# Kernel optimization log

Measured on AMD Instinct MI355X. Metric: run time of the kernel, lower is better.

The kernel has to match this reference:

```python
import jax, jax.numpy as jnp
import numpy as np

B, S, D, H = 2, 2048, 1024, 16
HD = D // H  # head_dim = 64
ROPE_BASE = 10000.0


def setup_inputs() -> dict:
    key = jax.random.key(0)
    ks = jax.random.split(key, 5)
    scale = 1.0 / np.sqrt(D)
    return {
        "x": jax.random.normal(ks[0], (B, S, D), dtype=jnp.float32),
        "Wq": jax.random.normal(ks[1], (D, D), dtype=jnp.float32) * scale,
        "Wk": jax.random.normal(ks[2], (D, D), dtype=jnp.float32) * scale,
        "Wv": jax.random.normal(ks[3], (D, D), dtype=jnp.float32) * scale,
        "Wo": jax.random.normal(ks[4], (D, D), dtype=jnp.float32) * scale,
    }


def _rotate_half(x):
    x1, x2 = x[..., : HD // 2], x[..., HD // 2:]
    return jnp.concatenate((-x2, x1), axis=-1)


def _rope_cos_sin(seq_len):
    inv_freq = 1.0 / (ROPE_BASE ** (jnp.arange(0, HD, 2, dtype=jnp.float32) / HD))
    t = jnp.arange(seq_len, dtype=jnp.float32)
    freqs = jnp.outer(t, inv_freq)          # [S, HD/2]
    emb = jnp.concatenate((freqs, freqs), -1)  # [S, HD]
    return jnp.cos(emb), jnp.sin(emb)


def reference(x, Wq, Wk, Wv, Wo):
    # projections (torch Linear: y = x @ W.T), split heads -> [B, H, S, HD]
    def proj(W):
        return (x @ W.T).reshape(B, S, H, HD).transpose(0, 2, 1, 3)

    q, k, v = proj(Wq), proj(Wk), proj(Wv)

    cos, sin = _rope_cos_sin(S)  # [S, HD] each, broadcast over B, H
    q = q * cos + _rotate_half(q) * sin
    k = k * cos + _rotate_half(k) * sin

    scale = 1.0 / np.sqrt(HD)
    scores = jnp.einsum("bhsd,bhtd->bhst", q, k) * scale  # [B,H,S,S]
    attn = jax.nn.softmax(scores, axis=-1)
    out = jnp.einsum("bhst,bhtd->bhsd", attn, v)           # [B,H,S,HD]
    out = out.transpose(0, 2, 1, 3).reshape(B, S, D)
    return out @ Wo.T
```

## Files before the change

kernel.cpp:

```cpp
#include <hip/hip_runtime.h>
#include <hip/hip_bf16.h>
#include <math.h>
#include <stdint.h>

typedef __bf16 bf16;
typedef __bf16 bf16x8 __attribute__((ext_vector_type(8)));
typedef __bf16 bf16x4 __attribute__((ext_vector_type(4)));
typedef float  f32x4  __attribute__((ext_vector_type(4)));

#define MFMA16(a,b,c) __builtin_amdgcn_mfma_f32_16x16x32_bf16((a),(b),(c),0,0,0)
#define GLOAD_LDS16(g, l) \
  __builtin_amdgcn_global_load_lds((__attribute__((address_space(1))) void*)(g), \
                                   (__attribute__((address_space(3))) void*)(l), 16, 0, 0)

static constexpr int kB  = 2;
static constexpr int kS  = 2048;
static constexpr int kD  = 1024;
static constexpr int kH  = 16;
static constexpr int kHD = 64;
static constexpr int kM  = kB * kS;
static constexpr float kExpC = 0.125f * 1.44269504f;

__global__ void cvt_all(const float* __restrict__ x,
                        const float* __restrict__ wq, const float* __restrict__ wk,
                        const float* __restrict__ wv, const float* __restrict__ wo,
                        bf16* __restrict__ xb,
                        bf16* __restrict__ wqb, bf16* __restrict__ wkb,
                        bf16* __restrict__ wvb, bf16* __restrict__ wob,
                        float2* __restrict__ rtab)
{
  const int i = blockIdx.x * 256 + threadIdx.x;
  const int NX4 = (kM * kD) / 4;
  const int NW4 = (kD * kD) / 4;
  if (i >= NX4 + 4 * NW4) {
    const int idx = i - (NX4 + 4 * NW4);
    const int s = idx >> 5, d = idx & 31;
    const float f = exp2f(-(float)d * 0.4152410118609203f);
    float sn, cs;
    sincosf((float)s * f, &sn, &cs);
    rtab[idx] = make_float2(cs, sn);
    return;
  }
  const float* src; bf16* dst; int off;
  if (i < NX4) { src = x; dst = xb; off = i; }
  else {
    const int j = i - NX4;
    const int seg = j >> 18;
    off = j & (NW4 - 1);
    src = (seg == 0) ? wq : (seg == 1) ? wk : (seg == 2) ? wv : wo;
    dst = (seg == 0) ? wqb : (seg == 1) ? wkb : (seg == 2) ? wvb : wob;
  }
  const float4 v = ((const float4*)src)[off];
  bf16x4 o = { (bf16)v.x, (bf16)v.y, (bf16)v.z, (bf16)v.w };
  ((bf16x4*)dst)[off] = o;
}

__device__ __forceinline__ void gemm_core_128(
    const bf16* __restrict__ A, const bf16* __restrict__ Bw,
    int m0, int n0, int K, bf16* aT, bf16* bT, f32x4 acc[4][4])
{
  const int t = threadIdx.x, lane = t & 63, wave = t >> 6;
  const int wm = wave >> 1, wn = wave & 1;
  const int srow = lane >> 2;
  const int scol = (lane & 3) * 8;
  for (int k0 = 0; k0 < K; k0 += 32) {
    __syncthreads();
#pragma unroll
    for (int c = 0; c < 2; ++c) {
      const int row = c * 64 + wave * 16 + srow;
      const bf16* ga = A  + (size_t)(m0 + row) * K + k0 + scol;
      const bf16* gb = Bw + (size_t)(n0 + row) * K + k0 + scol;
      GLOAD_LDS16(ga, aT + c * 2048 + wave * 512);
      GLOAD_LDS16(gb, bT + c * 2048 + wave * 512);
    }
    __syncthreads();
    bf16x8 af[4], bfr[4];
#pragma unroll
    for (int i = 0; i < 4; ++i) {
      af[i]  = *(const bf16x8*)(aT + (wm * 64 + i * 16 + (lane & 15)) * 32 + (lane >> 4) * 8);
      bfr[i] = *(const bf16x8*)(bT + (wn * 64 + i * 16 + (lane & 15)) * 32 + (lane >> 4) * 8);
    }
#pragma unroll
    for (int i = 0; i < 4; ++i)
#pragma unroll
      for (int j = 0; j < 4; ++j)
        acc[i][j] = MFMA16(af[i], bfr[j], acc[i][j]);
  }
}

__global__ __launch_bounds__(256) void proj_qkv(
    const bf16* __restrict__ xb,
    const bf16* __restrict__ wqb, const bf16* __restrict__ wkb, const bf16* __restrict__ wvb,
    bf16* __restrict__ Qb, bf16* __restrict__ Kb, bf16* __restrict__ Vb,
    const float2* __restrict__ rtab)
{
  __shared__ __align__(16) bf16 aT[4096];
  __shared__ __align__(16) bf16 bT[4096];
  const int z = blockIdx.z;
  const bf16* Ww = (z == 0) ? wqb : (z == 1) ? wkb : wvb;
  bf16*       Op = (z == 0) ? Qb  : (z == 1) ? Kb  : Vb;
  const int m0 = blockIdx.x * 128, n0 = blockIdx.y * 128;
  f32x4 acc[4][4] = {};
  gemm_core_128(xb, Ww, m0, n0, kD, aT, bT, acc);

  const int lane = threadIdx.x & 63, wave = threadIdx.x >> 6;
  const int wm = wave >> 1, wn = wave & 1, quad = lane >> 4, lc = lane & 15;
  const int hh = (n0 >> 6) + wn;
  if (z == 2) {
#pragma unroll
    for (int i = 0; i < 4; ++i)
#pragma unroll
      for (int r = 0; r < 4; ++r) {
        const int m = m0 + wm * 64 + i * 16 + quad * 4 + r;
        const int bidx = m >> 11, s = m & 2047;
        bf16* dst = Op + ((size_t)(bidx * kH + hh) * kS + s) * kHD;
#pragma unroll
        for (int j = 0; j < 4; ++j) dst[j * 16 + lc] = (bf16)acc[i][j][r];
      }
  } else {
#pragma unroll
    for (int j = 0; j < 2; ++j) {
      const int d = j * 16 + lc;
#pragma unroll
      for (int i = 0; i < 4; ++i)
#pragma unroll
        for (int r = 0; r < 4; ++r) {
          const int m = m0 + wm * 64 + i * 16 + quad * 4 + r;
          const int bidx = m >> 11, s = m & 2047;
          const float2 cs = rtab[s * 32 + d];
          const float v0 = acc[i][j][r], v1 = acc[i][j + 2][r];
          bf16* dst = Op + ((size_t)(bidx * kH + hh) * kS + s) * kHD;
          dst[d]      = (bf16)(v0 * cs.x - v1 * cs.y);
          dst[d + 32] = (bf16)(v1 * cs.x + v0 * cs.y);
        }
    }
  }
}

__global__ __launch_bounds__(256, 2) void attn(
    const bf16* __restrict__ Qb, const bf16* __restrict__ Kb,
    const bf16* __restrict__ Vb, bf16* __restrict__ Ob)
{
  __shared__ __align__(16) bf16 kT[128 * 72];
  __shared__ __align__(16) bf16 vT[64 * 136];
  __shared__ __align__(16) bf16 pT[4][32 * 136];
  const int t = threadIdx.x, lane = t & 63, wave = t >> 6;
  const int quad = lane >> 4, lc = lane & 15;
  const int qt = blockIdx.x, bh = blockIdx.y;
  const size_t base = (size_t)bh * kS * kHD;
  const bf16* Qp = Qb + base + (size_t)qt * 128 * kHD;
  const bf16* Kp = Kb + base;
  const bf16* Vp = Vb + base;

  bf16x8 qf[2][2];
#pragma unroll
  for (int tm = 0; tm < 2; ++tm)
#pragma unroll
    for (int ks = 0; ks < 2; ++ks)
      qf[tm][ks] = *(const bf16x8*)(Qp + (wave * 32 + tm * 16 + lc) * kHD + ks * 32 + quad * 8);

  f32x4 oacc[2][4] = {};
  f32x4 lacc[2] = {};
  const bf16 one = (bf16)1.0f;
  const bf16x8 ones = { one, one, one, one, one, one, one, one };

  const int srow = t >> 1;
  const int shalf = (t & 1) * 32;

  for (int kt = 0; kt < kS / 128; ++kt) {
    __syncthreads();
    {
      const bf16* ksrc = Kp + (size_t)(kt * 128 + srow) * kHD + shalf;
#pragma unroll
      for (int u = 0; u < 4; ++u)
        *(uint4*)&kT[srow * 72 + shalf + u * 8] = *(const uint4*)(ksrc + u * 8);
      const bf16* vsrc = Vp + (size_t)(kt * 128 + srow) * kHD + shalf;
      bf16 tmp[32];
#pragma unroll
      for (int u = 0; u < 4; ++u)
        *(uint4*)&tmp[u * 8] = *(const uint4*)(vsrc + u * 8);
#pragma unroll
      for (int e = 0; e < 32; ++e)
        vT[(shalf + e) * 136 + srow] = tmp[e];
    }
    __syncthreads();

    f32x4 sc[2][8] = {};
#pragma unroll
    for (int nk = 0; nk < 8; ++nk) {
      const bf16x8 kf0 = *(const bf16x8*)&kT[(nk * 16 + lc) * 72 + quad * 8];
      const bf16x8 kf1 = *(const bf16x8*)&kT[(nk * 16 + lc) * 72 + 32 + quad * 8];
#pragma unroll
      for (int tm = 0; tm < 2; ++tm) {
        sc[tm][nk] = MFMA16(qf[tm][0], kf0, sc[tm][nk]);
        sc[tm][nk] = MFMA16(qf[tm][1], kf1, sc[tm][nk]);
      }
    }

    bf16* pw = &pT[wave][0];
#pragma unroll
    for (int tm = 0; tm < 2; ++tm)
#pragma unroll
      for (int nk = 0; nk < 8; ++nk)
#pragma unroll
        for (int r = 0; r < 4; ++r) {
          const float p = __builtin_amdgcn_exp2f(sc[tm][nk][r] * kExpC);
          pw[(tm * 16 + quad * 4 + r) * 136 + nk * 16 + lc] = (bf16)p;
        }

    bf16x8 pf[2][4];
#pragma unroll
    for (int tm = 0; tm < 2; ++tm)
#pragma unroll
      for (int ks = 0; ks < 4; ++ks)
        pf[tm][ks] = *(const bf16x8*)&pw[(tm * 16 + lc) * 136 + ks * 32 + quad * 8];
#pragma unroll
    for (int ks = 0; ks < 4; ++ks)
#pragma unroll
      for (int tm = 0; tm < 2; ++tm)
        lacc[tm] = MFMA16(pf[tm][ks], ones, lacc[tm]);
#pragma unroll
    for (int nd = 0; nd < 4; ++nd)
#pragma unroll
      for (int ks = 0; ks < 4; ++ks) {
        const bf16x8 vf = *(const bf16x8*)&vT[(nd * 16 + lc) * 136 + ks * 32 + quad * 8];
#pragma unroll
        for (int tm = 0; tm < 2; ++tm)
          oacc[tm][nd] = MFMA16(pf[tm][ks], vf, oacc[tm][nd]);
      }
  }

  const int b = bh >> 4, h = bh & 15;
#pragma unroll
  for (int tm = 0; tm < 2; ++tm)
#pragma unroll
    for (int r = 0; r < 4; ++r) {
      const float inv = 1.0f / lacc[tm][r];
      const int s = qt * 128 + wave * 32 + tm * 16 + quad * 4 + r;
      bf16* dst = Ob + ((size_t)(b * kS + s)) * kD + h * kHD;
#pragma unroll
      for (int nd = 0; nd < 4; ++nd)
        dst[nd * 16 + lc] = (bf16)(oacc[tm][nd][r] * inv);
    }
}

__global__ __launch_bounds__(256) void out_proj(
    const bf16* __restrict__ Ab, const bf16* __restrict__ wob, float* __restrict__ Cout)
{
  __shared__ __align__(16) bf16 aT[4096];
  __shared__ __align__(16) bf16 bT[4096];
  const int m0 = blockIdx.x * 128, n0 = blockIdx.y * 128;
  f32x4 acc[4][4] = {};
  gemm_core_128(Ab, wob, m0, n0, kD, aT, bT, acc);
  const int lane = threadIdx.x & 63, wave = threadIdx.x >> 6;
  const int wm = wave >> 1, wn = wave & 1, quad = lane >> 4, lc = lane & 15;
#pragma unroll
  for (int i = 0; i < 4; ++i)
#pragma unroll
    for (int r = 0; r < 4; ++r) {
      const int m = m0 + wm * 64 + i * 16 + quad * 4 + r;
#pragma unroll
      for (int j = 0; j < 4; ++j)
        Cout[(size_t)m * kD + n0 + wn * 64 + j * 16 + lc] = acc[i][j][r];
    }
}

extern "C" void kernel_launch(void* const* d_in, const int* in_sizes, int n_in,
                              void* d_out, int out_size, void* d_ws, size_t ws_size,
                              hipStream_t stream)
{
  const float* x  = (const float*)d_in[0];
  const float* wq = (const float*)d_in[1];
  const float* wk = (const float*)d_in[2];
  const float* wv = (const float*)d_in[3];
  const float* wo = (const float*)d_in[4];
  float* out = (float*)d_out;

  char* ws = (char*)d_ws;
  const size_t MB = 1024 * 1024;
  if (ws_size < 49 * MB) return;
  bf16* xb  = (bf16*)(ws + 0 * MB);
  bf16* wqb = (bf16*)(ws + 8 * MB);
  bf16* wkb = (bf16*)(ws + 10 * MB);
  bf16* wvb = (bf16*)(ws + 12 * MB);
  bf16* wob = (bf16*)(ws + 14 * MB);
  bf16* Qb  = (bf16*)(ws + 16 * MB);
  bf16* Kb  = (bf16*)(ws + 24 * MB);
  bf16* Vb  = (bf16*)(ws + 32 * MB);
  bf16* Ob  = (bf16*)(ws + 40 * MB);
  float2* rtab = (float2*)(ws + 48 * MB);

  cvt_all<<<8448, 256, 0, stream>>>(x, wq, wk, wv, wo, xb, wqb, wkb, wvb, wob, rtab);
  proj_qkv<<<dim3(32, 8, 3), 256, 0, stream>>>(xb, wqb, wkb, wvb, Qb, Kb, Vb, rtab);
  attn<<<dim3(16, 32), 256, 0, stream>>>(Qb, Kb, Vb, Ob);
  out_proj<<<dim3(32, 8), 256, 0, stream>>>(Ob, wob, out);
}
```

Baseline: 215.8 us.

## Pre-transpose V in a separate kernel, fold softmax scale into Q, swap MFMA operands

Adds a transpose_v kernel that writes V as [bh, HD, S] so the attention loop loads V tiles with straight 16-byte copies instead of a 32-element scalar scatter transpose into LDS. The softmax scale times log2(e) is folded into Q at projection time, removing a multiply per score. The QK MFMA operands are swapped so each lane holds 4 consecutive keys and can store P as one bf16x4 vector instead of scalar stores. The cost is one extra kernel launch plus an extra read and write of V through a new 8 MB workspace region.

```diff
diff --git a/kernel.cpp b/kernel.cpp
--- a/kernel.cpp
+++ b/kernel.cpp
@@ -118,6 +118,7 @@
         for (int j = 0; j < 4; ++j) dst[j * 16 + lc] = (bf16)acc[i][j][r];
       }
   } else {
+    const float f = (z == 0) ? kExpC : 1.0f;
 #pragma unroll
     for (int j = 0; j < 2; ++j) {
       const int d = j * 16 + lc;
@@ -130,16 +131,42 @@
           const float2 cs = rtab[s * 32 + d];
           const float v0 = acc[i][j][r], v1 = acc[i][j + 2][r];
           bf16* dst = Op + ((size_t)(bidx * kH + hh) * kS + s) * kHD;
-          dst[d]      = (bf16)(v0 * cs.x - v1 * cs.y);
-          dst[d + 32] = (bf16)(v1 * cs.x + v0 * cs.y);
+          dst[d]      = (bf16)((v0 * cs.x - v1 * cs.y) * f);
+          dst[d + 32] = (bf16)((v1 * cs.x + v0 * cs.y) * f);
         }
     }
+  }
+}
+
+__global__ __launch_bounds__(256) void transpose_v(
+    const bf16* __restrict__ Vb, bf16* __restrict__ Vt)
+{
+  __shared__ __align__(16) bf16 buf[128 * 72];
+  const int t = threadIdx.x;
+  const int kc = blockIdx.x, bh = blockIdx.y;
+  const bf16* src = Vb + ((size_t)bh * kS + kc * 128) * kHD;
+  {
+    const int srow = t >> 1, half = (t & 1) * 32;
+#pragma unroll
+    for (int u = 0; u < 4; ++u)
+      *(uint4*)&buf[srow * 72 + half + u * 8] = *(const uint4*)(src + srow * kHD + half + u * 8);
+  }
+  __syncthreads();
+  {
+    const int d = t & 63, c = t >> 6;
+    bf16 tmp[32];
+#pragma unroll
+    for (int e = 0; e < 32; ++e) tmp[e] = buf[(c * 32 + e) * 72 + d];
+    bf16* dst = Vt + ((size_t)bh * kHD + d) * kS + kc * 128 + c * 32;
+#pragma unroll
+    for (int u = 0; u < 4; ++u)
+      *(uint4*)(dst + u * 8) = *(const uint4*)&tmp[u * 8];
   }
 }
 
 __global__ __launch_bounds__(256, 2) void attn(
     const bf16* __restrict__ Qb, const bf16* __restrict__ Kb,
-    const bf16* __restrict__ Vb, bf16* __restrict__ Ob)
+    const bf16* __restrict__ Vt, bf16* __restrict__ Ob)
 {
   __shared__ __align__(16) bf16 kT[128 * 72];
   __shared__ __align__(16) bf16 vT[64 * 136];
@@ -150,7 +177,7 @@
   const size_t base = (size_t)bh * kS * kHD;
   const bf16* Qp = Qb + base + (size_t)qt * 128 * kHD;
   const bf16* Kp = Kb + base;
-  const bf16* Vp = Vb + base;
+  const bf16* Vp = Vt + base;
 
   bf16x8 qf[2][2];
 #pragma unroll
@@ -164,8 +191,8 @@
   const bf16 one = (bf16)1.0f;
   const bf16x8 ones = { one, one, one, one, one, one, one, one };
 
-  const int srow = t >> 1;
-  const int shalf = (t & 1) * 32;
+  const int srow = t >> 1, shalf = (t & 1) * 32;
+  const int vd = t >> 2, vc = t & 3;
 
   for (int kt = 0; kt < kS / 128; ++kt) {
     __syncthreads();
@@ -174,14 +201,10 @@
 #pragma unroll
       for (int u = 0; u < 4; ++u)
         *(uint4*)&kT[srow * 72 + shalf + u * 8] = *(const uint4*)(ksrc + u * 8);
-      const bf16* vsrc = Vp + (size_t)(kt * 128 + srow) * kHD + shalf;
-      bf16 tmp[32];
+      const bf16* vsrc = Vp + (size_t)vd * kS + kt * 128 + vc * 32;
 #pragma unroll
       for (int u = 0; u < 4; ++u)
-        *(uint4*)&tmp[u * 8] = *(const uint4*)(vsrc + u * 8);
-#pragma unroll
-      for (int e = 0; e < 32; ++e)
-        vT[(shalf + e) * 136 + srow] = tmp[e];
+        *(uint4*)&vT[vd * 136 + vc * 32 + u * 8] = *(const uint4*)(vsrc + u * 8);
     }
     __syncthreads();
 
@@ -192,8 +215,8 @@
       const bf16x8 kf1 = *(const bf16x8*)&kT[(nk * 16 + lc) * 72 + 32 + quad * 8];
 #pragma unroll
       for (int tm = 0; tm < 2; ++tm) {
-        sc[tm][nk] = MFMA16(qf[tm][0], kf0, sc[tm][nk]);
-        sc[tm][nk] = MFMA16(qf[tm][1], kf1, sc[tm][nk]);
+        sc[tm][nk] = MFMA16(kf0, qf[tm][0], sc[tm][nk]);
+        sc[tm][nk] = MFMA16(kf1, qf[tm][1], sc[tm][nk]);
       }
     }
 
@@ -201,12 +224,13 @@
 #pragma unroll
     for (int tm = 0; tm < 2; ++tm)
 #pragma unroll
-      for (int nk = 0; nk < 8; ++nk)
-#pragma unroll
-        for (int r = 0; r < 4; ++r) {
-          const float p = __builtin_amdgcn_exp2f(sc[tm][nk][r] * kExpC);
-          pw[(tm * 16 + quad * 4 + r) * 136 + nk * 16 + lc] = (bf16)p;
-        }
+      for (int nk = 0; nk < 8; ++nk) {
+        bf16x4 p;
+#pragma unroll
+        for (int r = 0; r < 4; ++r)
+          p[r] = (bf16)__builtin_amdgcn_exp2f(sc[tm][nk][r]);
+        *(bf16x4*)&pw[(tm * 16 + lc) * 136 + nk * 16 + quad * 4] = p;
+      }
 
     bf16x8 pf[2][4];
 #pragma unroll
@@ -278,7 +302,7 @@
 
   char* ws = (char*)d_ws;
   const size_t MB = 1024 * 1024;
-  if (ws_size < 49 * MB) return;
+  if (ws_size < 57 * MB) return;
   bf16* xb  = (bf16*)(ws + 0 * MB);
   bf16* wqb = (bf16*)(ws + 8 * MB);
   bf16* wkb = (bf16*)(ws + 10 * MB);
@@ -289,9 +313,11 @@
   bf16* Vb  = (bf16*)(ws + 32 * MB);
   bf16* Ob  = (bf16*)(ws + 40 * MB);
   float2* rtab = (float2*)(ws + 48 * MB);
+  bf16* Vtp = (bf16*)(ws + 49 * MB);
 
   cvt_all<<<8448, 256, 0, stream>>>(x, wq, wk, wv, wo, xb, wqb, wkb, wvb, wob, rtab);
   proj_qkv<<<dim3(32, 8, 3), 256, 0, stream>>>(xb, wqb, wkb, wvb, Qb, Kb, Vb, rtab);
-  attn<<<dim3(16, 32), 256, 0, stream>>>(Qb, Kb, Vb, Ob);
+  transpose_v<<<dim3(16, 32), 256, 0, stream>>>(Vb, Vtp);
+  attn<<<dim3(16, 32), 256, 0, stream>>>(Qb, Kb, Vtp, Ob);
   out_proj<<<dim3(32, 8), 256, 0, stream>>>(Ob, wob, out);
 }
```

New measurement: 207.4 us. -3.9%, faster.
